# Optimization experiments

Hardware: AMD Instinct MI355X
Metric: run time of the kernel (lower is better)

## Reference

```python
import jax, jax.numpy as jnp
import numpy as np

N = 50000          # total particles (nodes)
E = 800000         # num edges
D = 256            # embed_dim
H = 8              # num_heads
ED = 6             # edge_dim
HD = D // H // 2   # head_dim = 16
LAMBDA_INIT = 1.0 - float(np.exp(-1.0))  # lambda_init_fn(depth=1)


def setup_inputs() -> dict:
    key = jax.random.key(0)
    ks = jax.random.split(key, 9)
    sc = lambda k, shape, fan_in: jax.random.normal(k, shape, jnp.float32) * (fan_in ** -0.5)
    x = jax.random.normal(ks[0], (N, D), jnp.float32)
    edge_index = jax.random.randint(ks[1], (2, E), 0, N, dtype=jnp.int64)
    edge_attr = jax.random.normal(ks[2], (E, ED), jnp.float32)
    v_w = sc(ks[3], (D, D), D)
    out_w = sc(ks[4], (D, D), D)
    e_w1 = sc(ks[5], (D, ED), ED)
    e_b1 = jnp.zeros((D,), jnp.float32)
    e_w2 = sc(ks[6], (2 * H, D), D)
    e_b2 = jnp.zeros((2 * H,), jnp.float32)
    lambda_q1 = 0.1 * jax.random.normal(ks[7], (100,), jnp.float32)
    lambda_k1 = 0.1 * jax.random.normal(ks[8], (100,), jnp.float32)
    return {"x": x, "edge_attr": edge_attr, "v_w": v_w, "out_w": out_w,
            "e_w1": e_w1, "e_b1": e_b1, "e_w2": e_w2, "e_b2": e_b2,
            "lambda_q1": lambda_q1, "lambda_k1": lambda_k1,
            "edge_index": edge_index}


def _scatter_softmax(scores, tgt, n):
    # numerically-stable segment softmax over edges grouped by tgt node
    m = jax.ops.segment_max(scores, tgt, num_segments=n)      # [n, H]
    e = jnp.exp(scores - m[tgt])                              # [E, H]
    s = jax.ops.segment_sum(e, tgt, num_segments=n)           # [n, H]
    return e / s[tgt]


def reference(x, edge_attr, v_w, out_w, e_w1, e_b1, e_w2, e_b2,
              lambda_q1, lambda_k1, edge_index):
    src, tgt = edge_index[0], edge_index[1]
    # V projection (no bias), split into heads of size 2*head_dim
    V = (x @ v_w.T).reshape(N, H, 2 * HD)
    # edge encoder MLP: Linear -> GELU(exact) -> Linear
    h = jax.nn.gelu(edge_attr @ e_w1.T + e_b1, approximate=False)
    edge_scores = (h @ e_w2.T + e_b2).reshape(E, H, 2)
    a1 = _scatter_softmax(edge_scores[:, :, 0], tgt, N)
    a2 = _scatter_softmax(edge_scores[:, :, 1], tgt, N)
    lambda_1 = jnp.exp(jnp.sum(lambda_q1 * lambda_k1))
    beta = jax.nn.sigmoid(lambda_1 * LAMBDA_INIT)
    attn_weights = a1 - beta * a2                              # [E, H]
    weighted_V = attn_weights[:, :, None] * V[src]             # [E, H, 2*HD]
    out = jax.ops.segment_sum(weighted_V, tgt, num_segments=N).reshape(N, D)
    out = out @ out_w.T
    return out, attn_weights, beta
```

## Files before the change

kernel.cpp:

```cpp
#include <hip/hip_runtime.h>
#include <hip/hip_bf16.h>
#include <math.h>

#define N_NODES 50000
#define N_EDGES 800000
#define DIM 256
#define HEADS 8
#define LAMBDA_INIT 0.63212055882855767f

using bf16x8 = __attribute__((ext_vector_type(8))) short;
using bf16x4 = __attribute__((ext_vector_type(4))) short;
using f32x4  = __attribute__((ext_vector_type(4))) float;
using f32x2  = __attribute__((ext_vector_type(2))) float;
#define MFMA16(a, b, c) __builtin_amdgcn_mfma_f32_16x16x32_bf16(a, b, c, 0, 0, 0)

__device__ __forceinline__ short f2b(float f) {
    __hip_bfloat16 h = __float2bfloat16(f);
    return *reinterpret_cast<short*>(&h);
}
__device__ __forceinline__ float b2f(short s) {
    unsigned u = ((unsigned)(unsigned short)s) << 16;
    return __uint_as_float(u);
}

__device__ __forceinline__ float gelu_f(float x) {
    float az = 0.70710678118654752f * fabsf(x);
    float t  = __builtin_amdgcn_rcpf(fmaf(0.47047f, az, 1.f));
    float q  = fmaf(fmaf(0.3739278f, t, -0.0479399f), t, 0.1740121f) * t;
    float E  = __expf(-az * az);
    return fmaf(-q * E, fabsf(x), fmaxf(x, 0.f));
}

__global__ void beta_kernel(const float* __restrict__ lq, const float* __restrict__ lk,
                            float* __restrict__ beta_ws, float* __restrict__ beta_out) {
    __shared__ float red[128];
    float v = 0.f;
    for (int i = threadIdx.x; i < 100; i += 128) v += lq[i] * lk[i];
    red[threadIdx.x] = v;
    __syncthreads();
    for (int s = 64; s > 0; s >>= 1) {
        if (threadIdx.x < s) red[threadIdx.x] += red[threadIdx.x + s];
        __syncthreads();
    }
    if (threadIdx.x == 0) {
        float l1 = expf(red[0]);
        float b = 1.f / (1.f + expf(-l1 * LAMBDA_INIT));
        *beta_ws = b;
        *beta_out = b;
    }
}

__global__ __launch_bounds__(256) void hist_kernel(const int* __restrict__ tgt,
                                                   int* __restrict__ cnt) {
    int e = blockIdx.x * 256 + threadIdx.x;
    if (e < N_EDGES) atomicAdd(&cnt[tgt[e]], 1);
}

__global__ __launch_bounds__(256) void scan1(const int* __restrict__ cnt,
                                             int* __restrict__ offs,
                                             int* __restrict__ partials, int n) {
    __shared__ int sh[256];
    int i = blockIdx.x * 256 + threadIdx.x;
    int v = (i < n) ? cnt[i] : 0;
    sh[threadIdx.x] = v;
    __syncthreads();
    for (int s = 1; s < 256; s <<= 1) {
        int add = (threadIdx.x >= s) ? sh[threadIdx.x - s] : 0;
        __syncthreads();
        sh[threadIdx.x] += add;
        __syncthreads();
    }
    if (i < n) offs[i] = sh[threadIdx.x] - v;
    if (threadIdx.x == 255) partials[blockIdx.x] = sh[255];
}

__global__ __launch_bounds__(256) void scan2(int* __restrict__ partials, int nb) {
    __shared__ int sh[256];
    int v = (threadIdx.x < nb) ? partials[threadIdx.x] : 0;
    sh[threadIdx.x] = v;
    __syncthreads();
    for (int s = 1; s < 256; s <<= 1) {
        int add = (threadIdx.x >= s) ? sh[threadIdx.x - s] : 0;
        __syncthreads();
        sh[threadIdx.x] += add;
        __syncthreads();
    }
    if (threadIdx.x < nb) partials[threadIdx.x] = sh[threadIdx.x] - v;
}

__global__ __launch_bounds__(256) void scan3(int* __restrict__ offs,
                                             const int* __restrict__ partials,
                                             int* __restrict__ cursor, int n) {
    int i = blockIdx.x * 256 + threadIdx.x;
    if (i < n) {
        int o = offs[i] + partials[blockIdx.x];
        offs[i] = o;
        cursor[i] = o;
    }
    if (i == 0) offs[n] = N_EDGES;
}

__global__ __launch_bounds__(256) void scatter_eid(const int* __restrict__ tgt,
                                                   int* __restrict__ cursor,
                                                   int* __restrict__ sorted_eid) {
    int e = blockIdx.x * 256 + threadIdx.x;
    if (e < N_EDGES) {
        int p = atomicAdd(&cursor[tgt[e]], 1);
        sorted_eid[p] = e;
    }
}

template <bool ABF, bool CBF>
__global__ __launch_bounds__(256) void gemm_mfma_t(const void* __restrict__ Av,
                                                   const float* __restrict__ W,
                                                   void* __restrict__ Cv, int M) {
    __shared__ __align__(16) short As[128 * 40];
    __shared__ __align__(16) short Ws[64 * 40];
    int tid = threadIdx.x;
    int lane = tid & 63, wv = tid >> 6;
    int l16 = lane & 15, quad = lane >> 4;
    int bm = blockIdx.x * 128, bn = blockIdx.y * 64;

    f32x4 acc[2][4];
#pragma unroll
    for (int mt = 0; mt < 2; ++mt)
#pragma unroll
        for (int nt = 0; nt < 4; ++nt) acc[mt][nt] = (f32x4){0.f, 0.f, 0.f, 0.f};

    int r = tid >> 1, hf = tid & 1;
    int rw = (tid & 127) >> 1, hw = tid & 1;

    for (int k0 = 0; k0 < 256; k0 += 32) {
        {
            int m = bm + r;
            bf16x8 p0, p1;
            if (ABF) {
                if (m < M) {
                    const bf16x8* ap =
                        (const bf16x8*)&((const short*)Av)[(size_t)m * 256 + k0 + hf * 16];
                    p0 = ap[0]; p1 = ap[1];
                } else {
                    p0 = (bf16x8){0,0,0,0,0,0,0,0}; p1 = p0;
                }
            } else {
                float4 f0, f1, f2, f3;
                if (m < M) {
                    const float4* ap =
                        (const float4*)&((const float*)Av)[(size_t)m * 256 + k0 + hf * 16];
                    f0 = ap[0]; f1 = ap[1]; f2 = ap[2]; f3 = ap[3];
                } else {
                    f0 = f1 = f2 = f3 = make_float4(0.f, 0.f, 0.f, 0.f);
                }
                p0[0]=f2b(f0.x); p0[1]=f2b(f0.y); p0[2]=f2b(f0.z); p0[3]=f2b(f0.w);
                p0[4]=f2b(f1.x); p0[5]=f2b(f1.y); p0[6]=f2b(f1.z); p0[7]=f2b(f1.w);
                p1[0]=f2b(f2.x); p1[1]=f2b(f2.y); p1[2]=f2b(f2.z); p1[3]=f2b(f2.w);
                p1[4]=f2b(f3.x); p1[5]=f2b(f3.y); p1[6]=f2b(f3.z); p1[7]=f2b(f3.w);
            }
            *(bf16x8*)&As[r * 40 + hf * 16]     = p0;
            *(bf16x8*)&As[r * 40 + hf * 16 + 8] = p1;
        }
        if (tid < 128) {
            const float4* wp = (const float4*)&W[(size_t)(bn + rw) * 256 + k0 + hw * 16];
            float4 f0 = wp[0], f1 = wp[1], f2 = wp[2], f3 = wp[3];
            bf16x8 p0, p1;
            p0[0]=f2b(f0.x); p0[1]=f2b(f0.y); p0[2]=f2b(f0.z); p0[3]=f2b(f0.w);
            p0[4]=f2b(f1.x); p0[5]=f2b(f1.y); p0[6]=f2b(f1.z); p0[7]=f2b(f1.w);
            p1[0]=f2b(f2.x); p1[1]=f2b(f2.y); p1[2]=f2b(f2.z); p1[3]=f2b(f2.w);
            p1[4]=f2b(f3.x); p1[5]=f2b(f3.y); p1[6]=f2b(f3.z); p1[7]=f2b(f3.w);
            *(bf16x8*)&Ws[rw * 40 + hw * 16]     = p0;
            *(bf16x8*)&Ws[rw * 40 + hw * 16 + 8] = p1;
        }
        __syncthreads();
#pragma unroll
        for (int mt = 0; mt < 2; ++mt) {
            bf16x8 afr = *(bf16x8*)&As[(wv * 32 + mt * 16 + l16) * 40 + quad * 8];
#pragma unroll
            for (int nt = 0; nt < 4; ++nt) {
                bf16x8 bfr = *(bf16x8*)&Ws[(nt * 16 + l16) * 40 + quad * 8];
                acc[mt][nt] = MFMA16(afr, bfr, acc[mt][nt]);
            }
        }
        __syncthreads();
    }
#pragma unroll
    for (int mt = 0; mt < 2; ++mt) {
#pragma unroll
        for (int rr = 0; rr < 4; ++rr) {
            int m = bm + wv * 32 + mt * 16 + quad * 4 + rr;
            if (m < M) {
#pragma unroll
                for (int nt = 0; nt < 4; ++nt) {
                    if (CBF)
                        ((short*)Cv)[(size_t)m * 256 + bn + nt * 16 + l16] =
                            f2b(acc[mt][nt][rr]);
                    else
                        ((float*)Cv)[(size_t)m * 256 + bn + nt * 16 + l16] =
                            acc[mt][nt][rr];
                }
            }
        }
    }
}

__global__ __launch_bounds__(256) void edge_mlp_mfma(const float* __restrict__ edge_attr,
                                                     const float* __restrict__ e_w1,
                                                     const float* __restrict__ e_b1,
                                                     const float* __restrict__ e_w2,
                                                     const float* __restrict__ e_b2,
                                                     float* __restrict__ scores) {
    __shared__ __align__(16) short w1s[256 * 8];
    __shared__ __align__(16) float b1s[256];
    __shared__ __align__(16) float ea_s[256 * 6];

    int tid = threadIdx.x;
    int lane = tid & 63, wv = tid >> 6;
    int l16 = lane & 15, quad = lane >> 4;

    {
        int n = tid;
#pragma unroll
        for (int k = 0; k < 6; ++k) w1s[n * 8 + k] = f2b(e_w1[n * 6 + k]);
        w1s[n * 8 + 6] = 0; w1s[n * 8 + 7] = 0;
        b1s[n] = e_b1[n];
    }
    {
        size_t base = (size_t)blockIdx.x * (256 * 6);
#pragma unroll
        for (int it = 0; it < 6; ++it) {
            int i = tid + it * 256;
            ea_s[i] = edge_attr[base + i];
        }
    }

    bf16x8 w2f[8];
#pragma unroll
    for (int c = 0; c < 8; ++c) {
#pragma unroll
        for (int j = 0; j < 8; ++j) {
            int col = c * 32 + ((j & 4) ? 16 : 0) + quad * 4 + (j & 3);
            w2f[c][j] = f2b(e_w2[l16 * 256 + col]);
        }
    }
    float b2r = e_b2[l16];
    __syncthreads();

    bf16x8 bfr[4];
#pragma unroll
    for (int g = 0; g < 4; ++g) {
        bfr[g] = (bf16x8){0, 0, 0, 0, 0, 0, 0, 0};
        if (quad == 0) {
            const float* p = &ea_s[(wv * 64 + g * 16 + l16) * 6];
#pragma unroll
            for (int j = 0; j < 6; ++j) bfr[g][j] = f2b(p[j]);
        }
    }

    f32x4 acc[4];
#pragma unroll
    for (int g = 0; g < 4; ++g) acc[g] = (f32x4){0.f, 0.f, 0.f, 0.f};

#pragma unroll
    for (int c2 = 0; c2 < 8; ++c2) {
        bf16x8 af0 = (bf16x8){0, 0, 0, 0, 0, 0, 0, 0};
        bf16x8 af1 = (bf16x8){0, 0, 0, 0, 0, 0, 0, 0};
        if (quad == 0) {
            af0 = *(bf16x8*)&w1s[((2 * c2) * 16 + l16) * 8];
            af1 = *(bf16x8*)&w1s[((2 * c2 + 1) * 16 + l16) * 8];
        }
        f32x4 bb0 = *(const f32x4*)&b1s[(2 * c2) * 16 + quad * 4];
        f32x4 bb1 = *(const f32x4*)&b1s[(2 * c2 + 1) * 16 + quad * 4];
#pragma unroll
        for (int g = 0; g < 4; ++g) {
            f32x4 cc0 = MFMA16(af0, bfr[g], bb0);
            f32x4 cc1 = MFMA16(af1, bfr[g], bb1);
            bf16x8 pa;
#pragma unroll
            for (int rr = 0; rr < 4; ++rr) {
                pa[rr]     = f2b(gelu_f(cc0[rr]));
                pa[4 + rr] = f2b(gelu_f(cc1[rr]));
            }
            acc[g] = MFMA16(pa, w2f[c2], acc[g]);
        }
    }

    long eblk = (long)blockIdx.x * 256 + wv * 64;
#pragma unroll
    for (int g = 0; g < 4; ++g) {
        long e0 = eblk + g * 16;
#pragma unroll
        for (int rr = 0; rr < 4; ++rr)
            scores[(size_t)(e0 + quad * 4 + rr) * 16 + l16] = acc[g][rr] + b2r;
    }
}

__global__ __launch_bounds__(256) void node_agg3(const int* __restrict__ sorted_eid,
                                                 const int* __restrict__ offs,
                                                 const int* __restrict__ srcp,
                                                 const float* __restrict__ scores,
                                                 const short* __restrict__ Vb,
                                                 const float* __restrict__ betap,
                                                 short* __restrict__ accumb,
                                                 float* __restrict__ attn_out) {
    __shared__ __align__(16) float scr_all[4][16 * 65];
    __shared__ __align__(16) float ms_all[4][32];
    __shared__ int src_all[4][64];

    int tid = threadIdx.x;
    int wv = tid >> 6, lane = tid & 63;
    int n = blockIdx.x * 4 + wv;
    float* scr = scr_all[wv];
    float* ms  = ms_all[wv];
    int* srcs  = src_all[wv];

    int beg = offs[n];
    int deg = offs[n + 1] - beg;
    int c16 = lane & 15, q4 = lane >> 4;
    int d0 = lane * 4, hh = lane >> 3;

    if (deg == 0) {
        bf16x4 z = (bf16x4){0, 0, 0, 0};
        *(bf16x4*)&accumb[(size_t)n * 256 + d0] = z;
        return;
    }
    float beta = *betap;

    if (deg <= 64) {
        int k = lane;
        int eid = 0, src = 0;
        float sc[16];
        if (k < deg) {
            eid = sorted_eid[beg + k];
            src = srcp[eid];
            const f32x4* sp = (const f32x4*)&scores[(size_t)eid * 16];
            f32x4 s0 = sp[0], s1 = sp[1], s2 = sp[2], s3 = sp[3];
            sc[0]=s0[0]; sc[1]=s0[1]; sc[2]=s0[2]; sc[3]=s0[3];
            sc[4]=s1[0]; sc[5]=s1[1]; sc[6]=s1[2]; sc[7]=s1[3];
            sc[8]=s2[0]; sc[9]=s2[1]; sc[10]=s2[2]; sc[11]=s2[3];
            sc[12]=s3[0]; sc[13]=s3[1]; sc[14]=s3[2]; sc[15]=s3[3];
        } else {
#pragma unroll
            for (int c = 0; c < 16; ++c) sc[c] = -INFINITY;
        }
        srcs[k] = src;
#pragma unroll
        for (int c = 0; c < 16; ++c) scr[c * 65 + k] = sc[c];

        float mloc = -INFINITY;
        for (int j = 0; 4 * j < deg; ++j)
            mloc = fmaxf(mloc, scr[c16 * 65 + 4 * j + q4]);
        mloc = fmaxf(mloc, __shfl_xor(mloc, 16));
        mloc = fmaxf(mloc, __shfl_xor(mloc, 32));
        float sloc = 0.f;
        for (int j = 0; 4 * j < deg; ++j)
            sloc += __expf(scr[c16 * 65 + 4 * j + q4] - mloc);
        sloc += __shfl_xor(sloc, 16);
        sloc += __shfl_xor(sloc, 32);
        if (lane < 16) {
            ms[c16] = mloc;
            ms[16 + c16] = __builtin_amdgcn_rcpf(sloc);
        }

        if (k < deg) {
            float w[8];
#pragma unroll
            for (int h = 0; h < 8; ++h) {
                f32x2 mp = *(const f32x2*)&ms[2 * h];
                f32x2 rp = *(const f32x2*)&ms[16 + 2 * h];
                w[h] = __expf(sc[2 * h] - mp[0]) * rp[0]
                     - beta * __expf(sc[2 * h + 1] - mp[1]) * rp[1];
            }
            f32x4 w0 = (f32x4){w[0], w[1], w[2], w[3]};
            f32x4 w1 = (f32x4){w[4], w[5], w[6], w[7]};
            *(f32x4*)&attn_out[(size_t)eid * 8]     = w0;
            *(f32x4*)&attn_out[(size_t)eid * 8 + 4] = w1;
            *(f32x4*)&scr[k * 8]     = w0;
            *(f32x4*)&scr[k * 8 + 4] = w1;
        }

        float a0 = 0.f, a1 = 0.f, a2 = 0.f, a3 = 0.f;
        for (int kk = 0; kk < deg; ++kk) {
            float wk = scr[kk * 8 + hh];
            int sk = srcs[kk];
            bf16x4 v = *(const bf16x4*)&Vb[(size_t)sk * 256 + d0];
            a0 += wk * b2f(v[0]);
            a1 += wk * b2f(v[1]);
            a2 += wk * b2f(v[2]);
            a3 += wk * b2f(v[3]);
        }
        bf16x4 r;
        r[0] = f2b(a0); r[1] = f2b(a1); r[2] = f2b(a2); r[3] = f2b(a3);
        *(bf16x4*)&accumb[(size_t)n * 256 + d0] = r;
        return;
    }

    float m_run = -INFINITY, s_run = 0.f;
    for (int base = 0; base < deg; base += 64) {
        int k = base + lane;
        float sc[16];
        if (k < deg) {
            int eid = sorted_eid[beg + k];
            const f32x4* sp = (const f32x4*)&scores[(size_t)eid * 16];
            f32x4 s0 = sp[0], s1 = sp[1], s2 = sp[2], s3 = sp[3];
            sc[0]=s0[0]; sc[1]=s0[1]; sc[2]=s0[2]; sc[3]=s0[3];
            sc[4]=s1[0]; sc[5]=s1[1]; sc[6]=s1[2]; sc[7]=s1[3];
            sc[8]=s2[0]; sc[9]=s2[1]; sc[10]=s2[2]; sc[11]=s2[3];
            sc[12]=s3[0]; sc[13]=s3[1]; sc[14]=s3[2]; sc[15]=s3[3];
        } else {
#pragma unroll
            for (int c = 0; c < 16; ++c) sc[c] = -INFINITY;
        }
#pragma unroll
        for (int c = 0; c < 16; ++c) scr[c * 65 + lane] = sc[c];
        float mc = -INFINITY;
#pragma unroll
        for (int j = 0; j < 16; ++j)
            mc = fmaxf(mc, scr[c16 * 65 + 4 * j + q4]);
        mc = fmaxf(mc, __shfl_xor(mc, 16));
        mc = fmaxf(mc, __shfl_xor(mc, 32));
        float m_new = fmaxf(m_run, mc);
        float ssum = 0.f;
#pragma unroll
        for (int j = 0; j < 16; ++j)
            ssum += __expf(scr[c16 * 65 + 4 * j + q4] - m_new);
        ssum += __shfl_xor(ssum, 16);
        ssum += __shfl_xor(ssum, 32);
        s_run = s_run * __expf(m_run - m_new) + ssum;
        m_run = m_new;
    }
    if (lane < 16) {
        ms[c16] = m_run;
        ms[16 + c16] = __builtin_amdgcn_rcpf(s_run);
    }

    float a0 = 0.f, a1 = 0.f, a2 = 0.f, a3 = 0.f;
    for (int base = 0; base < deg; base += 64) {
        int k = base + lane;
        int cn = min(64, deg - base);
        int src = 0;
        if (lane < cn) {
            int eid = sorted_eid[beg + k];
            src = srcp[eid];
            const f32x4* sp = (const f32x4*)&scores[(size_t)eid * 16];
            f32x4 s0 = sp[0], s1 = sp[1], s2 = sp[2], s3 = sp[3];
            float sc[16];
            sc[0]=s0[0]; sc[1]=s0[1]; sc[2]=s0[2]; sc[3]=s0[3];
            sc[4]=s1[0]; sc[5]=s1[1]; sc[6]=s1[2]; sc[7]=s1[3];
            sc[8]=s2[0]; sc[9]=s2[1]; sc[10]=s2[2]; sc[11]=s2[3];
            sc[12]=s3[0]; sc[13]=s3[1]; sc[14]=s3[2]; sc[15]=s3[3];
            float w[8];
#pragma unroll
            for (int h = 0; h < 8; ++h) {
                f32x2 mp = *(const f32x2*)&ms[2 * h];
                f32x2 rp = *(const f32x2*)&ms[16 + 2 * h];
                w[h] = __expf(sc[2 * h] - mp[0]) * rp[0]
                     - beta * __expf(sc[2 * h + 1] - mp[1]) * rp[1];
            }
            f32x4 w0 = (f32x4){w[0], w[1], w[2], w[3]};
            f32x4 w1 = (f32x4){w[4], w[5], w[6], w[7]};
            *(f32x4*)&attn_out[(size_t)eid * 8]     = w0;
            *(f32x4*)&attn_out[(size_t)eid * 8 + 4] = w1;
            *(f32x4*)&scr[lane * 8]     = w0;
            *(f32x4*)&scr[lane * 8 + 4] = w1;
        }
        srcs[lane] = src;
        for (int kk = 0; kk < cn; ++kk) {
            float wk = scr[kk * 8 + hh];
            int sk = srcs[kk];
            bf16x4 v = *(const bf16x4*)&Vb[(size_t)sk * 256 + d0];
            a0 += wk * b2f(v[0]);
            a1 += wk * b2f(v[1]);
            a2 += wk * b2f(v[2]);
            a3 += wk * b2f(v[3]);
        }
    }
    bf16x4 r;
    r[0] = f2b(a0); r[1] = f2b(a1); r[2] = f2b(a2); r[3] = f2b(a3);
    *(bf16x4*)&accumb[(size_t)n * 256 + d0] = r;
}

extern "C" void kernel_launch(void* const* d_in, const int* in_sizes, int n_in,
                              void* d_out, int out_size, void* d_ws, size_t ws_size,
                              hipStream_t stream) {
    const float* x         = (const float*)d_in[0];
    const float* edge_attr = (const float*)d_in[1];
    const float* v_w       = (const float*)d_in[2];
    const float* out_w     = (const float*)d_in[3];
    const float* e_w1      = (const float*)d_in[4];
    const float* e_b1      = (const float*)d_in[5];
    const float* e_w2      = (const float*)d_in[6];
    const float* e_b2      = (const float*)d_in[7];
    const float* lq        = (const float*)d_in[8];
    const float* lk        = (const float*)d_in[9];
    const int*   ei        = (const int*)d_in[10];
    const int* srcp = ei;
    const int* tgtp = ei + N_EDGES;

    float* out = (float*)d_out;
    float* attn_out = out + (size_t)N_NODES * 256;
    float* beta_out = attn_out + (size_t)N_EDGES * 8;

    short* Vb     = (short*)d_ws;
    float* scores = (float*)(Vb + (size_t)N_NODES * 256);
    short* accumb = (short*)(scores + (size_t)N_EDGES * 16);
    int*   cnt    = (int*)(accumb + (size_t)N_NODES * 256);
    int*   offs   = cnt + N_NODES;
    int*   cursor = offs + N_NODES + 1;
    int*   partials = cursor + N_NODES;
    int*   sorted_eid = partials + 256;
    float* betap  = (float*)(sorted_eid + N_EDGES);

    const int NB = (N_NODES + 255) / 256;

    beta_kernel<<<1, 128, 0, stream>>>(lq, lk, betap, beta_out);

    hipMemsetAsync(cnt, 0, N_NODES * sizeof(int), stream);
    hist_kernel<<<(N_EDGES + 255) / 256, 256, 0, stream>>>(tgtp, cnt);
    scan1<<<NB, 256, 0, stream>>>(cnt, offs, partials, N_NODES);
    scan2<<<1, 256, 0, stream>>>(partials, NB);
    scan3<<<NB, 256, 0, stream>>>(offs, partials, cursor, N_NODES);
    scatter_eid<<<(N_EDGES + 255) / 256, 256, 0, stream>>>(tgtp, cursor, sorted_eid);

    gemm_mfma_t<false, true><<<dim3((N_NODES + 127) / 128, 4), 256, 0, stream>>>(
        x, v_w, Vb, N_NODES);

    edge_mlp_mfma<<<N_EDGES / 256, 256, 0, stream>>>(edge_attr, e_w1, e_b1, e_w2, e_b2,
                                                     scores);

    node_agg3<<<N_NODES / 4, 256, 0, stream>>>(sorted_eid, offs, srcp, scores, Vb, betap,
                                               accumb, attn_out);

    gemm_mfma_t<true, false><<<dim3((N_NODES + 127) / 128, 4), 256, 0, stream>>>(
        accumb, out_w, out, N_NODES);
}
```

Measured before the change: 492.4 us.

## Fuse histogram into edge MLP, use GELU lookup table, fold beta into scan

The target-degree histogram atomics move into the edge MLP kernel, and the beta computation moves into scan2. Together these remove two kernel launches. Inside the edge MLP, the polynomial GELU is replaced with a per-block 1025-entry shared-memory table built with linear interpolation, and the bf16 packing now uses v_cvt_pk_bf16_f32. Every block rebuilds the table, which adds shared memory and setup work per block, and the table lowers GELU accuracy outside its clamp range and between grid points.

```diff
diff --git a/kernel.cpp b/kernel.cpp
--- a/kernel.cpp
+++ b/kernel.cpp
@@ -22,38 +22,22 @@
     unsigned u = ((unsigned)(unsigned short)s) << 16;
     return __uint_as_float(u);
 }
-
-__device__ __forceinline__ float gelu_f(float x) {
-    float az = 0.70710678118654752f * fabsf(x);
-    float t  = __builtin_amdgcn_rcpf(fmaf(0.47047f, az, 1.f));
-    float q  = fmaf(fmaf(0.3739278f, t, -0.0479399f), t, 0.1740121f) * t;
-    float E  = __expf(-az * az);
-    return fmaf(-q * E, fabsf(x), fmaxf(x, 0.f));
-}
-
-__global__ void beta_kernel(const float* __restrict__ lq, const float* __restrict__ lk,
-                            float* __restrict__ beta_ws, float* __restrict__ beta_out) {
-    __shared__ float red[128];
-    float v = 0.f;
-    for (int i = threadIdx.x; i < 100; i += 128) v += lq[i] * lk[i];
-    red[threadIdx.x] = v;
-    __syncthreads();
-    for (int s = 64; s > 0; s >>= 1) {
-        if (threadIdx.x < s) red[threadIdx.x] += red[threadIdx.x + s];
-        __syncthreads();
-    }
-    if (threadIdx.x == 0) {
-        float l1 = expf(red[0]);
-        float b = 1.f / (1.f + expf(-l1 * LAMBDA_INIT));
-        *beta_ws = b;
-        *beta_out = b;
-    }
-}
-
-__global__ __launch_bounds__(256) void hist_kernel(const int* __restrict__ tgt,
-                                                   int* __restrict__ cnt) {
-    int e = blockIdx.x * 256 + threadIdx.x;
-    if (e < N_EDGES) atomicAdd(&cnt[tgt[e]], 1);
+__device__ __forceinline__ unsigned cvt_pk_bf16(float a, float b) {
+    unsigned r;
+    asm("v_cvt_pk_bf16_f32 %0, %1, %2" : "=v"(r) : "v"(a), "v"(b));
+    return r;
+}
+
+__device__ __forceinline__ float fast_erf(float z) {
+    float az = fabsf(z);
+    float t = __builtin_amdgcn_rcpf(1.f + 0.3275911f * az);
+    float p = ((((1.061405429f * t - 1.453152027f) * t + 1.421413741f) * t
+                - 0.284496736f) * t + 0.254829592f) * t;
+    float e = 1.f - p * __expf(-az * az);
+    return copysignf(e, z);
+}
+__device__ __forceinline__ float gelu_exact(float x) {
+    return 0.5f * x * (1.f + fast_erf(0.70710678118654752f * x));
 }
 
 __global__ __launch_bounds__(256) void scan1(const int* __restrict__ cnt,
@@ -74,18 +58,41 @@
     if (threadIdx.x == 255) partials[blockIdx.x] = sh[255];
 }
 
-__global__ __launch_bounds__(256) void scan2(int* __restrict__ partials, int nb) {
+__global__ __launch_bounds__(256) void scan2(int* __restrict__ partials, int nb,
+                                             const float* __restrict__ lq,
+                                             const float* __restrict__ lk,
+                                             float* __restrict__ beta_ws,
+                                             float* __restrict__ beta_out) {
     __shared__ int sh[256];
-    int v = (threadIdx.x < nb) ? partials[threadIdx.x] : 0;
-    sh[threadIdx.x] = v;
+    __shared__ float redb[128];
+    int tid = threadIdx.x;
+    int v = (tid < nb) ? partials[tid] : 0;
+    sh[tid] = v;
     __syncthreads();
     for (int s = 1; s < 256; s <<= 1) {
-        int add = (threadIdx.x >= s) ? sh[threadIdx.x - s] : 0;
-        __syncthreads();
-        sh[threadIdx.x] += add;
-        __syncthreads();
-    }
-    if (threadIdx.x < nb) partials[threadIdx.x] = sh[threadIdx.x] - v;
+        int add = (tid >= s) ? sh[tid - s] : 0;
+        __syncthreads();
+        sh[tid] += add;
+        __syncthreads();
+    }
+    if (tid < nb) partials[tid] = sh[tid] - v;
+
+    if (tid < 128) {
+        float b = 0.f;
+        for (int i = tid; i < 100; i += 128) b += lq[i] * lk[i];
+        redb[tid] = b;
+    }
+    __syncthreads();
+    for (int s = 64; s > 0; s >>= 1) {
+        if (tid < s) redb[tid] += redb[tid + s];
+        __syncthreads();
+    }
+    if (tid == 0) {
+        float l1 = expf(redb[0]);
+        float b = 1.f / (1.f + expf(-l1 * LAMBDA_INIT));
+        *beta_ws = b;
+        *beta_out = b;
+    }
 }
 
 __global__ __launch_bounds__(256) void scan3(int* __restrict__ offs,
@@ -207,15 +214,28 @@
                                                      const float* __restrict__ e_b1,
                                                      const float* __restrict__ e_w2,
                                                      const float* __restrict__ e_b2,
-                                                     float* __restrict__ scores) {
+                                                     float* __restrict__ scores,
+                                                     const int* __restrict__ tgt,
+                                                     int* __restrict__ cnt) {
     __shared__ __align__(16) short w1s[256 * 8];
     __shared__ __align__(16) float b1s[256];
     __shared__ __align__(16) float ea_s[256 * 6];
+    __shared__ __align__(16) float tab[1025 * 2 + 2];
 
     int tid = threadIdx.x;
     int lane = tid & 63, wv = tid >> 6;
     int l16 = lane & 15, quad = lane >> 4;
 
+    atomicAdd(&cnt[tgt[blockIdx.x * 256 + tid]], 1);
+
+    for (int idx = tid; idx < 1025; idx += 256) {
+        float xx = (float)idx * 0.015625f - 8.f;
+        float t0 = gelu_exact(xx);
+        float t1 = gelu_exact(xx + 0.015625f);
+        tab[idx * 2] = t0;
+        tab[idx * 2 + 1] = t1 - t0;
+    }
+
     {
         int n = tid;
 #pragma unroll
@@ -243,6 +263,16 @@
     }
     float b2r = e_b2[l16];
     __syncthreads();
+
+    auto gelu_t = [&](float x) -> float {
+        float xc = fminf(fmaxf(x, -8.f), 7.984375f);
+        float z = fmaf(xc, 64.f, 512.f);
+        int i = (int)z;
+        float f = z - (float)i;
+        f32x2 td = *(const f32x2*)&tab[i * 2];
+        float h = fmaf(f, td[1], td[0]);
+        return (x > 7.984375f) ? x : h;
+    };
 
     bf16x8 bfr[4];
 #pragma unroll
@@ -273,12 +303,12 @@
         for (int g = 0; g < 4; ++g) {
             f32x4 cc0 = MFMA16(af0, bfr[g], bb0);
             f32x4 cc1 = MFMA16(af1, bfr[g], bb1);
-            bf16x8 pa;
-#pragma unroll
-            for (int rr = 0; rr < 4; ++rr) {
-                pa[rr]     = f2b(gelu_f(cc0[rr]));
-                pa[4 + rr] = f2b(gelu_f(cc1[rr]));
-            }
+            unsigned pw[4];
+            pw[0] = cvt_pk_bf16(gelu_t(cc0[0]), gelu_t(cc0[1]));
+            pw[1] = cvt_pk_bf16(gelu_t(cc0[2]), gelu_t(cc0[3]));
+            pw[2] = cvt_pk_bf16(gelu_t(cc1[0]), gelu_t(cc1[1]));
+            pw[3] = cvt_pk_bf16(gelu_t(cc1[2]), gelu_t(cc1[3]));
+            bf16x8 pa = *reinterpret_cast<bf16x8*>(pw);
             acc[g] = MFMA16(pa, w2f[c2], acc[g]);
         }
     }
@@ -511,21 +541,19 @@
 
     const int NB = (N_NODES + 255) / 256;
 
-    beta_kernel<<<1, 128, 0, stream>>>(lq, lk, betap, beta_out);
-
     hipMemsetAsync(cnt, 0, N_NODES * sizeof(int), stream);
-    hist_kernel<<<(N_EDGES + 255) / 256, 256, 0, stream>>>(tgtp, cnt);
+
+    edge_mlp_mfma<<<N_EDGES / 256, 256, 0, stream>>>(edge_attr, e_w1, e_b1, e_w2, e_b2,
+                                                     scores, tgtp, cnt);
+
     scan1<<<NB, 256, 0, stream>>>(cnt, offs, partials, N_NODES);
-    scan2<<<1, 256, 0, stream>>>(partials, NB);
+    scan2<<<1, 256, 0, stream>>>(partials, NB, lq, lk, betap, beta_out);
     scan3<<<NB, 256, 0, stream>>>(offs, partials, cursor, N_NODES);
     scatter_eid<<<(N_EDGES + 255) / 256, 256, 0, stream>>>(tgtp, cursor, sorted_eid);
 
     gemm_mfma_t<false, true><<<dim3((N_NODES + 127) / 128, 4), 256, 0, stream>>>(
         x, v_w, Vb, N_NODES);
 
-    edge_mlp_mfma<<<N_EDGES / 256, 256, 0, stream>>>(edge_attr, e_w1, e_b1, e_w2, e_b2,
-                                                     scores);
-
     node_agg3<<<N_NODES / 4, 256, 0, stream>>>(sorted_eid, offs, srcp, scores, Vb, betap,
                                                accumb, attn_out);
 
```

New measurement: 438.3 us. 11.0% less time.
